# Kernel optimization log

Measured on AMD Instinct MI355X. Metric: run time of the kernel, lower is better.

## Reference

```python
import jax, jax.numpy as jnp
import numpy as np
import math

B, N, D, H, CD = 2, 384, 256, 8, 3
HD = D // H

def _linear_init(key, out_f, in_f):
    k1, k2 = jax.random.split(key)
    bound = 1.0 / math.sqrt(in_f)
    w = jax.random.uniform(k1, (out_f, in_f), jnp.float32, -bound, bound)
    b = jax.random.uniform(k2, (out_f,), jnp.float32, -bound, bound)
    return w, b

def setup_inputs() -> dict:
    key = jax.random.key(0)
    ks = jax.random.split(key, 7)
    x = jax.random.normal(ks[0], (B, N, D), jnp.float32)
    coords = jax.random.normal(ks[1], (B, N, CD), jnp.float32)
    qkv_w, qkv_b = _linear_init(ks[2], 3 * D, D)
    rb_w1, rb_b1 = _linear_init(ks[3], D, CD)
    rb_w2, rb_b2 = _linear_init(ks[4], H, D)
    rv_w1, rv_b1 = _linear_init(ks[5], D, CD)
    rv_w2, rv_b2 = _linear_init(ks[6], D, D)
    return {"x": x, "coords": coords, "qkv_w": qkv_w, "qkv_b": qkv_b,
            "rb_w1": rb_w1, "rb_b1": rb_b1, "rb_w2": rb_w2, "rb_b2": rb_b2,
            "rv_w1": rv_w1, "rv_b1": rv_b1, "rv_w2": rv_w2, "rv_b2": rv_b2}

def reference(x, coords, qkv_w, qkv_b, rb_w1, rb_b1, rb_w2, rb_b2, rv_w1, rv_b1, rv_w2, rv_b2):
    # QKV projection -> (B, H, N, HD) each
    qkv = x @ qkv_w.T + qkv_b
    q, k, v = jnp.split(qkv, 3, axis=-1)
    to_heads = lambda t: t.reshape(B, N, H, HD).transpose(0, 2, 1, 3)
    qh, kh, vh = to_heads(q), to_heads(k), to_heads(v)

    # pairwise relative coordinates: (B, N, N, CD)
    rel = coords[:, :, None, :] - coords[:, None, :, :]

    # rel_bias MLP: (B, N, N, H) -> (B, H, N, N)
    rel_bias = jax.nn.silu(rel @ rb_w1.T + rb_b1) @ rb_w2.T + rb_b2
    rel_bias = rel_bias.transpose(0, 3, 1, 2)

    # rel_value MLP: (B, N, N, D) -> (B, H, N, N, HD)
    rel_value = jax.nn.silu(rel @ rv_w1.T + rv_b1) @ rv_w2.T + rv_b2
    rel_value = rel_value.reshape(B, N, N, H, HD).transpose(0, 3, 1, 2, 4)

    # attn_mask=None path: all-true boolean mask -> additive term is zero
    scores = jnp.einsum('bhid,bhjd->bhij', qh, kh) / math.sqrt(float(HD)) + rel_bias
    weights = jax.nn.softmax(scores, axis=-1)

    base = jnp.einsum('bhij,bhjd->bhid', weights, vh)
    rel_context = jnp.einsum('bhij,bhijd->bhid', weights, rel_value)
    context = base + rel_context  # (B, H, N, HD)
    return context.transpose(0, 2, 1, 3).reshape(B, N, D)
```

## Files before the change

### kernel.cpp

```cpp
#include <hip/hip_runtime.h>
#include <math.h>

#define BB 2
#define NN 384
#define DD 256
#define HH 8
#define RN (BB * NN)
#define INV_SQRT_HD 0.17677669529663687f
#define LOG2E 1.4426950408889634f
#define NLN2 -0.6931471805599453f
#define QSCALE (INV_SQRT_HD * LOG2E)

#define W2_ST 264
#define T_ST  264
#define EB_ST 392

typedef float f32x4 __attribute__((ext_vector_type(4)));
typedef __bf16 bf16x8 __attribute__((ext_vector_type(8)));
typedef __bf16 bf16x4 __attribute__((ext_vector_type(4)));

__device__ __forceinline__ f32x4 mfma16(bf16x8 a, bf16x8 b, f32x4 c) {
    return __builtin_amdgcn_mfma_f32_16x16x32_bf16(a, b, c, 0, 0, 0);
}

__device__ __forceinline__ float hidp(float d) {
    float e = __builtin_amdgcn_exp2f(d);
    return d * __builtin_amdgcn_rcpf(1.0f + e);
}
__device__ __forceinline__ bf16x8 hid8(bf16x8 av, float4 a0, float4 a1) {
    bf16x8 r;
    r[0] = (__bf16)hidp((float)av[0] - a0.x);
    r[1] = (__bf16)hidp((float)av[1] - a0.y);
    r[2] = (__bf16)hidp((float)av[2] - a0.z);
    r[3] = (__bf16)hidp((float)av[3] - a0.w);
    r[4] = (__bf16)hidp((float)av[4] - a1.x);
    r[5] = (__bf16)hidp((float)av[5] - a1.y);
    r[6] = (__bf16)hidp((float)av[6] - a1.z);
    r[7] = (__bf16)hidp((float)av[7] - a1.w);
    return r;
}
__device__ __forceinline__ bf16x8 hid8s(bf16x8 av, float a) {
    bf16x8 r;
#pragma unroll
    for (int q = 0; q < 8; ++q) r[q] = (__bf16)hidp((float)av[q] - a);
    return r;
}
__device__ __forceinline__ bf16x8 pack8(float4 a, float4 b) {
    bf16x8 r;
    r[0] = (__bf16)a.x; r[1] = (__bf16)a.y; r[2] = (__bf16)a.z; r[3] = (__bf16)a.w;
    r[4] = (__bf16)b.x; r[5] = (__bf16)b.y; r[6] = (__bf16)b.z; r[7] = (__bf16)b.w;
    return r;
}
__device__ __forceinline__ float selv(f32x4 v, int r) {
    return (r == 0) ? v[0] : (r == 1) ? v[1] : (r == 2) ? v[2] : v[3];
}

__global__ __launch_bounds__(256) void prep_kernel(
    const float* __restrict__ x, const float* __restrict__ coords,
    const float* __restrict__ qkv_w, const float* __restrict__ qkv_b,
    const float* __restrict__ rb_w1, const float* __restrict__ rv_w1,
    const float* __restrict__ rb_w2,
    float* __restrict__ qb, __bf16* __restrict__ kbbf, __bf16* __restrict__ vT,
    __bf16* __restrict__ Arb, __bf16* __restrict__ ArvT,
    __bf16* __restrict__ w2neg)
{
    int bid = blockIdx.x, tid = threadIdx.x;
    if (bid >= 1344) {
        int idx = tid * 8;
        float4 wa = *(const float4*)(rb_w2 + idx);
        float4 wb = *(const float4*)(rb_w2 + idx + 4);
        float4 na = make_float4(-wa.x, -wa.y, -wa.z, -wa.w);
        float4 nb = make_float4(-wb.x, -wb.y, -wb.z, -wb.w);
        *(bf16x8*)(w2neg + idx) = pack8(na, nb);
        return;
    }
    if (bid >= 576) {
        int r = bid - 576, c = tid;
        float cx = coords[r * 3 + 0], cy = coords[r * 3 + 1], cz = coords[r * 3 + 2];
        float ab = (cx * rb_w1[c * 3] + cy * rb_w1[c * 3 + 1] + cz * rb_w1[c * 3 + 2]) * LOG2E;
        float av = (cx * rv_w1[c * 3] + cy * rv_w1[c * 3 + 1] + cz * rv_w1[c * 3 + 2]) * LOG2E;
        Arb[r * DD + c] = (__bf16)ab;
        ArvT[c * RN + r] = (__bf16)av;
        return;
    }
    int mt = bid % 48, nb = bid / 48;
    int w = tid >> 6, l = tid & 63, lr = l & 15, lg = l >> 4;
    int m0 = mt * 16, n0 = nb * 64 + w * 16;
    const float* xr = x + (size_t)(m0 + lr) * DD;
    const float* wr = qkv_w + (size_t)(n0 + lr) * DD;
    f32x4 acc = {0.f, 0.f, 0.f, 0.f};
#pragma unroll
    for (int ks = 0; ks < 8; ++ks) {
        int c0 = ks * 32 + lg * 8;
        float4 xa = *(const float4*)(xr + c0);
        float4 xb = *(const float4*)(xr + c0 + 4);
        float4 wa = *(const float4*)(wr + c0);
        float4 wb = *(const float4*)(wr + c0 + 4);
        acc = mfma16(pack8(xa, xb), pack8(wa, wb), acc);
    }
    int col = n0 + lr;
    float bo = qkv_b[col];
    int part = col >> 8, o = col & 255;
#pragma unroll
    for (int r = 0; r < 4; ++r) {
        int m = m0 + lg * 4 + r;
        float v = acc[r] + bo;
        if (part == 0) {
            qb[(size_t)m * DD + o] = v * QSCALE;
        } else if (part == 1) {
            kbbf[(size_t)m * DD + o] = (__bf16)v;
        } else {
            int b = (m >= NN) ? 1 : 0;
            int n = m - b * NN;
            vT[(size_t)b * DD * NN + (size_t)o * NN + n] = (__bf16)v;
        }
    }
}

__global__ __launch_bounds__(256, 4) void k2a_kernel(
    const float* __restrict__ rb_b1, const __bf16* __restrict__ w2neg,
    const float* __restrict__ rb_b2,
    const float* __restrict__ qb, const __bf16* __restrict__ kbbf,
    const __bf16* __restrict__ Arb,
    __bf16* __restrict__ eG, float* __restrict__ Zpart)
{
    __shared__ __align__(16) __bf16 qsbf[2][DD];
    __shared__ __align__(16) float Apr[2][DD];
    __shared__ __align__(16) __bf16 w2bf[HH * W2_ST];
    __shared__ float redsm[4][2][HH];

    int tid = threadIdx.x;
    int bid = blockIdx.x;
    int gp = bid >> 1, half = bid & 1;
    int gi0 = gp * 2;
    int b = (gp >= 192) ? 1 : 0;

    qsbf[0][tid] = (__bf16)qb[(size_t)gi0 * DD + tid];
    qsbf[1][tid] = (__bf16)qb[(size_t)(gi0 + 1) * DD + tid];
    float b1l = rb_b1[tid] * LOG2E;
    Apr[0][tid] = (float)Arb[(size_t)gi0 * DD + tid] + b1l;
    Apr[1][tid] = (float)Arb[(size_t)(gi0 + 1) * DD + tid] + b1l;
    {
        int idx = tid * 8;
        *(bf16x8*)&w2bf[(idx >> 8) * W2_ST + (idx & 255)] =
            *(const bf16x8*)(w2neg + idx);
    }
    __syncthreads();

    int l = tid & 63, wv = tid >> 6;
    int lr = l & 15, lg = l >> 4;
    float rb2l = rb_b2[lr & 7] * LOG2E;

    int jb0 = half * 192 + wv * 16;
    int jb1 = jb0 + 64, jb2 = jb0 + 128;
    const __bf16* arbB = Arb + (size_t)b * NN * DD;
    const __bf16* kbB  = kbbf + (size_t)b * NN * DD;
    const __bf16* ar0 = arbB + (size_t)(jb0 + lr) * DD;
    const __bf16* ar1 = arbB + (size_t)(jb1 + lr) * DD;
    const __bf16* ar2 = arbB + (size_t)(jb2 + lr) * DD;
    const __bf16* kr0 = kbB  + (size_t)(jb0 + lr) * DD;
    const __bf16* kr1 = kbB  + (size_t)(jb1 + lr) * DD;
    const __bf16* kr2 = kbB  + (size_t)(jb2 + lr) * DD;
    const __bf16* wfp = &w2bf[(lr & 7) * W2_ST];

    bf16x8 qf0_reg = *(const bf16x8*)&qsbf[0][(lr & 7) * 32 + lg * 8];
    bf16x8 qf1_reg = *(const bf16x8*)&qsbf[1][(lr & 7) * 32 + lg * 8];
    bf16x8 zero8;
#pragma unroll
    for (int e = 0; e < 8; ++e) zero8[e] = (__bf16)0.f;

    f32x4 zzz = {0.f, 0.f, 0.f, 0.f};
    f32x4 a00 = zzz, a01 = zzz, a02 = zzz;
    f32x4 a10 = zzz, a11 = zzz, a12 = zzz;
#pragma unroll
    for (int ks = 0; ks < 8; ++ks) {
        int c0 = ks * 32 + lg * 8;
        bf16x8 v0 = *(const bf16x8*)(ar0 + c0);
        bf16x8 v1 = *(const bf16x8*)(ar1 + c0);
        bf16x8 v2 = *(const bf16x8*)(ar2 + c0);
        bf16x8 k0 = *(const bf16x8*)(kr0 + c0);
        bf16x8 k1 = *(const bf16x8*)(kr1 + c0);
        bf16x8 k2 = *(const bf16x8*)(kr2 + c0);
        bf16x8 wf = *(const bf16x8*)(wfp + c0);
        float4 p00 = *(const float4*)&Apr[0][c0];
        float4 p01 = *(const float4*)&Apr[0][c0 + 4];
        float4 p10 = *(const float4*)&Apr[1][c0];
        float4 p11 = *(const float4*)&Apr[1][c0 + 4];
        bf16x8 q0 = (lr == ks) ? qf0_reg : zero8;
        bf16x8 q1 = (lr == ks) ? qf1_reg : zero8;
        a00 = mfma16(hid8(v0, p00, p01), wf, a00);
        a10 = mfma16(hid8(v0, p10, p11), wf, a10);
        a01 = mfma16(hid8(v1, p00, p01), wf, a01);
        a11 = mfma16(hid8(v1, p10, p11), wf, a11);
        a02 = mfma16(hid8(v2, p00, p01), wf, a02);
        a12 = mfma16(hid8(v2, p10, p11), wf, a12);
        a00 = mfma16(k0, q0, a00);
        a10 = mfma16(k0, q1, a10);
        a01 = mfma16(k1, q0, a01);
        a11 = mfma16(k1, q1, a11);
        a02 = mfma16(k2, q0, a02);
        a12 = mfma16(k2, q1, a12);
    }

    float z0 = 0.f, z1 = 0.f;
#define FINTILE(ACC, GI, JB, ZACC) { \
        float e0 = __builtin_amdgcn_exp2f(ACC[0] + rb2l); \
        float e1 = __builtin_amdgcn_exp2f(ACC[1] + rb2l); \
        float e2 = __builtin_amdgcn_exp2f(ACC[2] + rb2l); \
        float e3 = __builtin_amdgcn_exp2f(ACC[3] + rb2l); \
        if (lr < 8) { \
            bf16x4 ev; \
            ev[0] = (__bf16)e0; ev[1] = (__bf16)e1; \
            ev[2] = (__bf16)e2; ev[3] = (__bf16)e3; \
            *(bf16x4*)&eG[((size_t)(GI) * HH + lr) * NN + (JB) + lg * 4] = ev; \
        } \
        float zs = e0 + e1 + e2 + e3; \
        zs += __shfl_xor(zs, 16); \
        zs += __shfl_xor(zs, 32); \
        ZACC += zs; }
    FINTILE(a00, gi0,     jb0, z0)
    FINTILE(a01, gi0,     jb1, z0)
    FINTILE(a02, gi0,     jb2, z0)
    FINTILE(a10, gi0 + 1, jb0, z1)
    FINTILE(a11, gi0 + 1, jb1, z1)
    FINTILE(a12, gi0 + 1, jb2, z1)
#undef FINTILE
    if (lg == 0 && lr < 8) {
        redsm[wv][0][lr] = z0;
        redsm[wv][1][lr] = z1;
    }
    __syncthreads();
    if (tid < 16) {
        int g = tid >> 3, h = tid & 7;
        Zpart[((size_t)(gi0 + g) * 2 + half) * 8 + h] =
            redsm[0][g][h] + redsm[1][g][h] + redsm[2][g][h] + redsm[3][g][h];
    }
}

__global__ __launch_bounds__(256, 4) void k2b_kernel(
    const float* __restrict__ rv_b1, const float* __restrict__ rv_w2,
    const __bf16* __restrict__ vT, const __bf16* __restrict__ ArvT,
    const __bf16* __restrict__ eG,
    float* __restrict__ rcpart, float* __restrict__ basef)
{
    __shared__ __align__(16) float Apv[2][DD];
    __shared__ __align__(16) float Tl[2][HH * T_ST];
    __shared__ __align__(16) __bf16 els[16 * EB_ST];

    int tid = threadIdx.x;
    int bid = blockIdx.x;
    int gp = bid >> 1, ch = bid & 1;
    int gi0 = gp * 2;
    int b = (gp >= 192) ? 1 : 0;

    float b1l = rv_b1[tid] * LOG2E;
    Apv[0][tid] = (float)ArvT[(size_t)tid * RN + gi0] + b1l;
    Apv[1][tid] = (float)ArvT[(size_t)tid * RN + gi0 + 1] + b1l;
    {
        int r = tid >> 4, cg = tid & 15;
        const __bf16* src = eG + (size_t)(gi0 * 8 + r) * NN;
#pragma unroll
        for (int s = 0; s < 3; ++s) {
            int col = s * 128 + cg * 8;
            *(bf16x8*)&els[r * EB_ST + col] = *(const bf16x8*)(src + col);
        }
    }
    __syncthreads();

    int l = tid & 63, wv = tid >> 6;
    int lr = l & 15, lg = l >> 4;

    int c0 = ch * 128 + wv * 16 + lr;
    int c1 = c0 + 64;
    float ap00 = Apv[0][c0], ap01 = Apv[0][c1];
    float ap10 = Apv[1][c0], ap11 = Apv[1][c1];
    const __bf16* vr0 = ArvT + (size_t)c0 * RN + b * NN;
    const __bf16* vr1 = ArvT + (size_t)c1 * RN + b * NN;
    const __bf16* tv0 = vT + (size_t)b * DD * NN + (size_t)c0 * NN;
    const __bf16* tv1 = vT + (size_t)b * DD * NN + (size_t)c1 * NN;

    f32x4 zzz = {0.f, 0.f, 0.f, 0.f};
    f32x4 T00 = zzz, T01 = zzz, T10 = zzz, T11 = zzz;
    f32x4 B0 = zzz, B1 = zzz;
#pragma unroll
    for (int ks = 0; ks < 12; ++ks) {
        int j0 = ks * 32 + lg * 8;
        bf16x8 ef  = *(const bf16x8*)&els[lr * EB_ST + j0];
        bf16x8 av0 = *(const bf16x8*)(vr0 + j0);
        bf16x8 av1 = *(const bf16x8*)(vr1 + j0);
        bf16x8 w0  = *(const bf16x8*)(tv0 + j0);
        bf16x8 w1  = *(const bf16x8*)(tv1 + j0);
        T00 = mfma16(ef, hid8s(av0, ap00), T00);
        T01 = mfma16(ef, hid8s(av1, ap01), T01);
        T10 = mfma16(ef, hid8s(av0, ap10), T10);
        T11 = mfma16(ef, hid8s(av1, ap11), T11);
        B0  = mfma16(ef, w0, B0);
        B1  = mfma16(ef, w1, B1);
    }

    if (lg < 2) {
#pragma unroll
        for (int r = 0; r < 4; ++r) {
            int h = lg * 4 + r;
            Tl[0][h * T_ST + c0] = T00[r] * NLN2;
            Tl[0][h * T_ST + c1] = T01[r] * NLN2;
        }
    } else {
#pragma unroll
        for (int r = 0; r < 4; ++r) {
            int h = (lg - 2) * 4 + r;
            Tl[1][h * T_ST + c0] = T10[r] * NLN2;
            Tl[1][h * T_ST + c1] = T11[r] * NLN2;
        }
    }
    {
        int h0 = c0 >> 5;
        if (lg == (h0 >> 2))     basef[(size_t)gi0 * DD + c0]       = selv(B0, h0 & 3);
        if (lg == 2 + (h0 >> 2)) basef[(size_t)(gi0 + 1) * DD + c0] = selv(B0, h0 & 3);
        int h1 = c1 >> 5;
        if (lg == (h1 >> 2))     basef[(size_t)gi0 * DD + c1]       = selv(B1, h1 & 3);
        if (lg == 2 + (h1 >> 2)) basef[(size_t)(gi0 + 1) * DD + c1] = selv(B1, h1 & 3);
    }
    __syncthreads();

    {
        int o = tid, h = o >> 5;
        const float4* w2p = (const float4*)(rv_w2 + (size_t)o * DD);
        const float* t0 = &Tl[0][h * T_ST];
        const float* t1 = &Tl[1][h * T_ST];
        float a0 = 0.f, a1 = 0.f;
#pragma unroll 4
        for (int cc = 0; cc < 32; ++cc) {
            int cidx = ch * 32 + cc;
            float4 wv4 = w2p[cidx];
            float4 u0 = *(const float4*)&t0[cidx * 4];
            float4 u1 = *(const float4*)&t1[cidx * 4];
            a0 += wv4.x * u0.x + wv4.y * u0.y + wv4.z * u0.z + wv4.w * u0.w;
            a1 += wv4.x * u1.x + wv4.y * u1.y + wv4.z * u1.z + wv4.w * u1.w;
        }
        rcpart[((size_t)ch * RN + gi0) * DD + o] = a0;
        rcpart[((size_t)ch * RN + gi0 + 1) * DD + o] = a1;
    }
}

__global__ __launch_bounds__(256) void k2c_kernel(
    const float* __restrict__ rcpart, const float* __restrict__ basef,
    const float* __restrict__ Zpart, const float* __restrict__ rv_b2,
    float* __restrict__ out)
{
    int gi = blockIdx.x, o = threadIdx.x, h = o >> 5;
    float z = Zpart[(size_t)gi * 16 + h] + Zpart[(size_t)gi * 16 + 8 + h];
    float rc = rcpart[(size_t)gi * DD + o] + rcpart[((size_t)RN + gi) * DD + o];
    out[(size_t)gi * DD + o] =
        (rc + basef[(size_t)gi * DD + o]) * __builtin_amdgcn_rcpf(z) + rv_b2[o];
}

extern "C" void kernel_launch(void* const* d_in, const int* in_sizes, int n_in,
                              void* d_out, int out_size, void* d_ws, size_t ws_size,
                              hipStream_t stream) {
    const float* x      = (const float*)d_in[0];
    const float* coords = (const float*)d_in[1];
    const float* qkv_w  = (const float*)d_in[2];
    const float* qkv_b  = (const float*)d_in[3];
    const float* rb_w1  = (const float*)d_in[4];
    const float* rb_b1  = (const float*)d_in[5];
    const float* rb_w2  = (const float*)d_in[6];
    const float* rb_b2  = (const float*)d_in[7];
    const float* rv_w1  = (const float*)d_in[8];
    const float* rv_b1  = (const float*)d_in[9];
    const float* rv_w2  = (const float*)d_in[10];
    const float* rv_b2  = (const float*)d_in[11];
    float* out = (float*)d_out;

    float* ws = (float*)d_ws;
    const int PER = RN * DD;
    float* qb = ws;
    __bf16* bfb  = (__bf16*)(ws + PER);
    __bf16* kbbf = bfb;
    __bf16* vTb  = bfb + PER;
    __bf16* Arb  = bfb + 2 * PER;
    __bf16* ArvT = bfb + 3 * PER;
    __bf16* eG   = bfb + 4 * PER;
    float* Zpart = (float*)(eG + (size_t)RN * HH * NN);
    float* basef = Zpart + (size_t)RN * 2 * HH;
    float* rcpart = basef + PER;
    __bf16* w2neg = (__bf16*)(rcpart + 2 * (size_t)PER);

    prep_kernel<<<1345, 256, 0, stream>>>(x, coords, qkv_w, qkv_b,
                                          rb_w1, rv_w1, rb_w2,
                                          qb, kbbf, vTb, Arb, ArvT, w2neg);
    k2a_kernel<<<RN, 256, 0, stream>>>(rb_b1, w2neg, rb_b2,
                                       qb, kbbf, Arb, eG, Zpart);
    k2b_kernel<<<RN, 256, 0, stream>>>(rv_b1, rv_w2,
                                       vTb, ArvT, eG, rcpart, basef);
    k2c_kernel<<<RN, 256, 0, stream>>>(rcpart, basef, Zpart, rv_b2, out);
}
```

Baseline: 76.86 us.

## Fuse score and rel-value kernels, keeping exp weights in LDS per j-half

Merges the attention-score kernel and the rel-value/context kernel into one launch. Each block now keeps its unnormalised exp weights for its 192-key half in shared memory instead of writing them to global and reading them back. The second stage is re-split by key half rather than by output channel, so every block covers all 256 channels over its half of the keys. Per-half base and rel-context partials are summed in the final kernel. This removes one launch and the global round trip of the exp matrix, but each block does the full rv_w2 projection, uses more LDS and registers, and adds a row-major copy of the rel-value first-layer activations.

```diff
diff --git a/kernel.cpp b/kernel.cpp
--- a/kernel.cpp
+++ b/kernel.cpp
@@ -13,7 +13,7 @@
 
 #define W2_ST 264
 #define T_ST  264
-#define EB_ST 392
+#define ELST  200
 
 typedef float f32x4 __attribute__((ext_vector_type(4)));
 typedef __bf16 bf16x8 __attribute__((ext_vector_type(8)));
@@ -61,7 +61,7 @@
     const float* __restrict__ rb_w1, const float* __restrict__ rv_w1,
     const float* __restrict__ rb_w2,
     float* __restrict__ qb, __bf16* __restrict__ kbbf, __bf16* __restrict__ vT,
-    __bf16* __restrict__ Arb, __bf16* __restrict__ ArvT,
+    __bf16* __restrict__ Arb, __bf16* __restrict__ ArvT, __bf16* __restrict__ Arv,
     __bf16* __restrict__ w2neg)
 {
     int bid = blockIdx.x, tid = threadIdx.x;
@@ -81,6 +81,7 @@
         float av = (cx * rv_w1[c * 3] + cy * rv_w1[c * 3 + 1] + cz * rv_w1[c * 3 + 2]) * LOG2E;
         Arb[r * DD + c] = (__bf16)ab;
         ArvT[c * RN + r] = (__bf16)av;
+        Arv[r * DD + c] = (__bf16)av;
         return;
     }
     int mt = bid % 48, nb = bid / 48;
@@ -117,16 +118,22 @@
     }
 }
 
-__global__ __launch_bounds__(256, 4) void k2a_kernel(
+__global__ __launch_bounds__(256, 4) void k2ab_kernel(
     const float* __restrict__ rb_b1, const __bf16* __restrict__ w2neg,
-    const float* __restrict__ rb_b2,
+    const float* __restrict__ rb_b2, const float* __restrict__ rv_b1,
     const float* __restrict__ qb, const __bf16* __restrict__ kbbf,
-    const __bf16* __restrict__ Arb,
-    __bf16* __restrict__ eG, float* __restrict__ Zpart)
+    const __bf16* __restrict__ Arb, const __bf16* __restrict__ ArvT,
+    const __bf16* __restrict__ Arv, const __bf16* __restrict__ vT,
+    const float* __restrict__ rv_w2,
+    float* __restrict__ rcpart, float* __restrict__ basef,
+    float* __restrict__ Zpart)
 {
     __shared__ __align__(16) __bf16 qsbf[2][DD];
     __shared__ __align__(16) float Apr[2][DD];
+    __shared__ __align__(16) float Apv[2][DD];
     __shared__ __align__(16) __bf16 w2bf[HH * W2_ST];
+    __shared__ __align__(16) __bf16 els[16 * ELST];
+    __shared__ __align__(16) float Tl[2][HH * T_ST];
     __shared__ float redsm[4][2][HH];
 
     int tid = threadIdx.x;
@@ -137,9 +144,12 @@
 
     qsbf[0][tid] = (__bf16)qb[(size_t)gi0 * DD + tid];
     qsbf[1][tid] = (__bf16)qb[(size_t)(gi0 + 1) * DD + tid];
-    float b1l = rb_b1[tid] * LOG2E;
-    Apr[0][tid] = (float)Arb[(size_t)gi0 * DD + tid] + b1l;
-    Apr[1][tid] = (float)Arb[(size_t)(gi0 + 1) * DD + tid] + b1l;
+    float b1r = rb_b1[tid] * LOG2E;
+    Apr[0][tid] = (float)Arb[(size_t)gi0 * DD + tid] + b1r;
+    Apr[1][tid] = (float)Arb[(size_t)(gi0 + 1) * DD + tid] + b1r;
+    float b1v = rv_b1[tid] * LOG2E;
+    Apv[0][tid] = (float)Arv[(size_t)gi0 * DD + tid] + b1v;
+    Apv[1][tid] = (float)Arv[(size_t)(gi0 + 1) * DD + tid] + b1v;
     {
         int idx = tid * 8;
         *(bf16x8*)&w2bf[(idx >> 8) * W2_ST + (idx & 255)] =
@@ -151,59 +161,60 @@
     int lr = l & 15, lg = l >> 4;
     float rb2l = rb_b2[lr & 7] * LOG2E;
 
-    int jb0 = half * 192 + wv * 16;
-    int jb1 = jb0 + 64, jb2 = jb0 + 128;
-    const __bf16* arbB = Arb + (size_t)b * NN * DD;
-    const __bf16* kbB  = kbbf + (size_t)b * NN * DD;
-    const __bf16* ar0 = arbB + (size_t)(jb0 + lr) * DD;
-    const __bf16* ar1 = arbB + (size_t)(jb1 + lr) * DD;
-    const __bf16* ar2 = arbB + (size_t)(jb2 + lr) * DD;
-    const __bf16* kr0 = kbB  + (size_t)(jb0 + lr) * DD;
-    const __bf16* kr1 = kbB  + (size_t)(jb1 + lr) * DD;
-    const __bf16* kr2 = kbB  + (size_t)(jb2 + lr) * DD;
-    const __bf16* wfp = &w2bf[(lr & 7) * W2_ST];
-
-    bf16x8 qf0_reg = *(const bf16x8*)&qsbf[0][(lr & 7) * 32 + lg * 8];
-    bf16x8 qf1_reg = *(const bf16x8*)&qsbf[1][(lr & 7) * 32 + lg * 8];
-    bf16x8 zero8;
-#pragma unroll
-    for (int e = 0; e < 8; ++e) zero8[e] = (__bf16)0.f;
-
-    f32x4 zzz = {0.f, 0.f, 0.f, 0.f};
-    f32x4 a00 = zzz, a01 = zzz, a02 = zzz;
-    f32x4 a10 = zzz, a11 = zzz, a12 = zzz;
-#pragma unroll
-    for (int ks = 0; ks < 8; ++ks) {
-        int c0 = ks * 32 + lg * 8;
-        bf16x8 v0 = *(const bf16x8*)(ar0 + c0);
-        bf16x8 v1 = *(const bf16x8*)(ar1 + c0);
-        bf16x8 v2 = *(const bf16x8*)(ar2 + c0);
-        bf16x8 k0 = *(const bf16x8*)(kr0 + c0);
-        bf16x8 k1 = *(const bf16x8*)(kr1 + c0);
-        bf16x8 k2 = *(const bf16x8*)(kr2 + c0);
-        bf16x8 wf = *(const bf16x8*)(wfp + c0);
-        float4 p00 = *(const float4*)&Apr[0][c0];
-        float4 p01 = *(const float4*)&Apr[0][c0 + 4];
-        float4 p10 = *(const float4*)&Apr[1][c0];
-        float4 p11 = *(const float4*)&Apr[1][c0 + 4];
-        bf16x8 q0 = (lr == ks) ? qf0_reg : zero8;
-        bf16x8 q1 = (lr == ks) ? qf1_reg : zero8;
-        a00 = mfma16(hid8(v0, p00, p01), wf, a00);
-        a10 = mfma16(hid8(v0, p10, p11), wf, a10);
-        a01 = mfma16(hid8(v1, p00, p01), wf, a01);
-        a11 = mfma16(hid8(v1, p10, p11), wf, a11);
-        a02 = mfma16(hid8(v2, p00, p01), wf, a02);
-        a12 = mfma16(hid8(v2, p10, p11), wf, a12);
-        a00 = mfma16(k0, q0, a00);
-        a10 = mfma16(k0, q1, a10);
-        a01 = mfma16(k1, q0, a01);
-        a11 = mfma16(k1, q1, a11);
-        a02 = mfma16(k2, q0, a02);
-        a12 = mfma16(k2, q1, a12);
-    }
-
-    float z0 = 0.f, z1 = 0.f;
-#define FINTILE(ACC, GI, JB, ZACC) { \
+    {
+        int jl0 = wv * 16, jl1 = jl0 + 64, jl2 = jl0 + 128;
+        int jg0 = half * 192 + jl0;
+        const __bf16* arbB = Arb + (size_t)b * NN * DD;
+        const __bf16* kbB  = kbbf + (size_t)b * NN * DD;
+        const __bf16* ar0 = arbB + (size_t)(jg0 + lr) * DD;
+        const __bf16* ar1 = ar0 + (size_t)64 * DD;
+        const __bf16* ar2 = ar0 + (size_t)128 * DD;
+        const __bf16* kr0 = kbB + (size_t)(jg0 + lr) * DD;
+        const __bf16* kr1 = kr0 + (size_t)64 * DD;
+        const __bf16* kr2 = kr0 + (size_t)128 * DD;
+        const __bf16* wfp = &w2bf[(lr & 7) * W2_ST];
+
+        bf16x8 qf0_reg = *(const bf16x8*)&qsbf[0][(lr & 7) * 32 + lg * 8];
+        bf16x8 qf1_reg = *(const bf16x8*)&qsbf[1][(lr & 7) * 32 + lg * 8];
+        bf16x8 zero8;
+#pragma unroll
+        for (int e = 0; e < 8; ++e) zero8[e] = (__bf16)0.f;
+
+        f32x4 zzz = {0.f, 0.f, 0.f, 0.f};
+        f32x4 a00 = zzz, a01 = zzz, a02 = zzz;
+        f32x4 a10 = zzz, a11 = zzz, a12 = zzz;
+#pragma unroll
+        for (int ks = 0; ks < 8; ++ks) {
+            int c0 = ks * 32 + lg * 8;
+            bf16x8 v0 = *(const bf16x8*)(ar0 + c0);
+            bf16x8 v1 = *(const bf16x8*)(ar1 + c0);
+            bf16x8 v2 = *(const bf16x8*)(ar2 + c0);
+            bf16x8 k0 = *(const bf16x8*)(kr0 + c0);
+            bf16x8 k1 = *(const bf16x8*)(kr1 + c0);
+            bf16x8 k2 = *(const bf16x8*)(kr2 + c0);
+            bf16x8 wf = *(const bf16x8*)(wfp + c0);
+            float4 p00 = *(const float4*)&Apr[0][c0];
+            float4 p01 = *(const float4*)&Apr[0][c0 + 4];
+            float4 p10 = *(const float4*)&Apr[1][c0];
+            float4 p11 = *(const float4*)&Apr[1][c0 + 4];
+            bf16x8 q0 = (lr == ks) ? qf0_reg : zero8;
+            bf16x8 q1 = (lr == ks) ? qf1_reg : zero8;
+            a00 = mfma16(hid8(v0, p00, p01), wf, a00);
+            a10 = mfma16(hid8(v0, p10, p11), wf, a10);
+            a01 = mfma16(hid8(v1, p00, p01), wf, a01);
+            a11 = mfma16(hid8(v1, p10, p11), wf, a11);
+            a02 = mfma16(hid8(v2, p00, p01), wf, a02);
+            a12 = mfma16(hid8(v2, p10, p11), wf, a12);
+            a00 = mfma16(k0, q0, a00);
+            a10 = mfma16(k0, q1, a10);
+            a01 = mfma16(k1, q0, a01);
+            a11 = mfma16(k1, q1, a11);
+            a02 = mfma16(k2, q0, a02);
+            a12 = mfma16(k2, q1, a12);
+        }
+
+        float z0 = 0.f, z1 = 0.f;
+#define FINTILE(ACC, G, JL, ZACC) { \
         float e0 = __builtin_amdgcn_exp2f(ACC[0] + rb2l); \
         float e1 = __builtin_amdgcn_exp2f(ACC[1] + rb2l); \
         float e2 = __builtin_amdgcn_exp2f(ACC[2] + rb2l); \
@@ -212,22 +223,23 @@
             bf16x4 ev; \
             ev[0] = (__bf16)e0; ev[1] = (__bf16)e1; \
             ev[2] = (__bf16)e2; ev[3] = (__bf16)e3; \
-            *(bf16x4*)&eG[((size_t)(GI) * HH + lr) * NN + (JB) + lg * 4] = ev; \
+            *(bf16x4*)&els[((G) * 8 + lr) * ELST + (JL) + lg * 4] = ev; \
         } \
         float zs = e0 + e1 + e2 + e3; \
         zs += __shfl_xor(zs, 16); \
         zs += __shfl_xor(zs, 32); \
         ZACC += zs; }
-    FINTILE(a00, gi0,     jb0, z0)
-    FINTILE(a01, gi0,     jb1, z0)
-    FINTILE(a02, gi0,     jb2, z0)
-    FINTILE(a10, gi0 + 1, jb0, z1)
-    FINTILE(a11, gi0 + 1, jb1, z1)
-    FINTILE(a12, gi0 + 1, jb2, z1)
+        FINTILE(a00, 0, jl0, z0)
+        FINTILE(a01, 0, jl1, z0)
+        FINTILE(a02, 0, jl2, z0)
+        FINTILE(a10, 1, jl0, z1)
+        FINTILE(a11, 1, jl1, z1)
+        FINTILE(a12, 1, jl2, z1)
 #undef FINTILE
-    if (lg == 0 && lr < 8) {
-        redsm[wv][0][lr] = z0;
-        redsm[wv][1][lr] = z1;
+        if (lg == 0 && lr < 8) {
+            redsm[wv][0][lr] = z0;
+            redsm[wv][1][lr] = z1;
+        }
     }
     __syncthreads();
     if (tid < 16) {
@@ -235,91 +247,86 @@
         Zpart[((size_t)(gi0 + g) * 2 + half) * 8 + h] =
             redsm[0][g][h] + redsm[1][g][h] + redsm[2][g][h] + redsm[3][g][h];
     }
-}
-
-__global__ __launch_bounds__(256, 4) void k2b_kernel(
-    const float* __restrict__ rv_b1, const float* __restrict__ rv_w2,
-    const __bf16* __restrict__ vT, const __bf16* __restrict__ ArvT,
-    const __bf16* __restrict__ eG,
-    float* __restrict__ rcpart, float* __restrict__ basef)
-{
-    __shared__ __align__(16) float Apv[2][DD];
-    __shared__ __align__(16) float Tl[2][HH * T_ST];
-    __shared__ __align__(16) __bf16 els[16 * EB_ST];
-
-    int tid = threadIdx.x;
-    int bid = blockIdx.x;
-    int gp = bid >> 1, ch = bid & 1;
-    int gi0 = gp * 2;
-    int b = (gp >= 192) ? 1 : 0;
-
-    float b1l = rv_b1[tid] * LOG2E;
-    Apv[0][tid] = (float)ArvT[(size_t)tid * RN + gi0] + b1l;
-    Apv[1][tid] = (float)ArvT[(size_t)tid * RN + gi0 + 1] + b1l;
+
     {
-        int r = tid >> 4, cg = tid & 15;
-        const __bf16* src = eG + (size_t)(gi0 * 8 + r) * NN;
-#pragma unroll
-        for (int s = 0; s < 3; ++s) {
-            int col = s * 128 + cg * 8;
-            *(bf16x8*)&els[r * EB_ST + col] = *(const bf16x8*)(src + col);
-        }
-    }
-    __syncthreads();
-
-    int l = tid & 63, wv = tid >> 6;
-    int lr = l & 15, lg = l >> 4;
-
-    int c0 = ch * 128 + wv * 16 + lr;
-    int c1 = c0 + 64;
-    float ap00 = Apv[0][c0], ap01 = Apv[0][c1];
-    float ap10 = Apv[1][c0], ap11 = Apv[1][c1];
-    const __bf16* vr0 = ArvT + (size_t)c0 * RN + b * NN;
-    const __bf16* vr1 = ArvT + (size_t)c1 * RN + b * NN;
-    const __bf16* tv0 = vT + (size_t)b * DD * NN + (size_t)c0 * NN;
-    const __bf16* tv1 = vT + (size_t)b * DD * NN + (size_t)c1 * NN;
-
-    f32x4 zzz = {0.f, 0.f, 0.f, 0.f};
-    f32x4 T00 = zzz, T01 = zzz, T10 = zzz, T11 = zzz;
-    f32x4 B0 = zzz, B1 = zzz;
-#pragma unroll
-    for (int ks = 0; ks < 12; ++ks) {
-        int j0 = ks * 32 + lg * 8;
-        bf16x8 ef  = *(const bf16x8*)&els[lr * EB_ST + j0];
-        bf16x8 av0 = *(const bf16x8*)(vr0 + j0);
-        bf16x8 av1 = *(const bf16x8*)(vr1 + j0);
-        bf16x8 w0  = *(const bf16x8*)(tv0 + j0);
-        bf16x8 w1  = *(const bf16x8*)(tv1 + j0);
-        T00 = mfma16(ef, hid8s(av0, ap00), T00);
-        T01 = mfma16(ef, hid8s(av1, ap01), T01);
-        T10 = mfma16(ef, hid8s(av0, ap10), T10);
-        T11 = mfma16(ef, hid8s(av1, ap11), T11);
-        B0  = mfma16(ef, w0, B0);
-        B1  = mfma16(ef, w1, B1);
-    }
-
-    if (lg < 2) {
-#pragma unroll
-        for (int r = 0; r < 4; ++r) {
-            int h = lg * 4 + r;
-            Tl[0][h * T_ST + c0] = T00[r] * NLN2;
-            Tl[0][h * T_ST + c1] = T01[r] * NLN2;
-        }
-    } else {
-#pragma unroll
-        for (int r = 0; r < 4; ++r) {
-            int h = (lg - 2) * 4 + r;
-            Tl[1][h * T_ST + c0] = T10[r] * NLN2;
-            Tl[1][h * T_ST + c1] = T11[r] * NLN2;
-        }
-    }
-    {
-        int h0 = c0 >> 5;
-        if (lg == (h0 >> 2))     basef[(size_t)gi0 * DD + c0]       = selv(B0, h0 & 3);
-        if (lg == 2 + (h0 >> 2)) basef[(size_t)(gi0 + 1) * DD + c0] = selv(B0, h0 & 3);
-        int h1 = c1 >> 5;
-        if (lg == (h1 >> 2))     basef[(size_t)gi0 * DD + c1]       = selv(B1, h1 & 3);
-        if (lg == 2 + (h1 >> 2)) basef[(size_t)(gi0 + 1) * DD + c1] = selv(B1, h1 & 3);
+        int cc = wv * 16 + lr;
+        float ap00 = Apv[0][cc], ap01 = Apv[0][cc + 64];
+        float ap02 = Apv[0][cc + 128], ap03 = Apv[0][cc + 192];
+        float ap10 = Apv[1][cc], ap11 = Apv[1][cc + 64];
+        float ap12 = Apv[1][cc + 128], ap13 = Apv[1][cc + 192];
+        int joff = b * NN + half * 192;
+        const __bf16* vr0 = ArvT + (size_t)cc * RN + joff;
+        const __bf16* vr1 = ArvT + (size_t)(cc + 64) * RN + joff;
+        const __bf16* vr2 = ArvT + (size_t)(cc + 128) * RN + joff;
+        const __bf16* vr3 = ArvT + (size_t)(cc + 192) * RN + joff;
+        const __bf16* tvB = vT + (size_t)b * DD * NN + half * 192;
+        const __bf16* tv0 = tvB + (size_t)cc * NN;
+        const __bf16* tv1 = tvB + (size_t)(cc + 64) * NN;
+        const __bf16* tv2 = tvB + (size_t)(cc + 128) * NN;
+        const __bf16* tv3 = tvB + (size_t)(cc + 192) * NN;
+
+        f32x4 zzz = {0.f, 0.f, 0.f, 0.f};
+        f32x4 T00 = zzz, T01 = zzz, T02 = zzz, T03 = zzz;
+        f32x4 T10 = zzz, T11 = zzz, T12 = zzz, T13 = zzz;
+        f32x4 Bb0 = zzz, Bb1 = zzz, Bb2 = zzz, Bb3 = zzz;
+#pragma unroll
+        for (int ks = 0; ks < 6; ++ks) {
+            int j0 = ks * 32 + lg * 8;
+            bf16x8 ef  = *(const bf16x8*)&els[lr * ELST + j0];
+            bf16x8 av0 = *(const bf16x8*)(vr0 + j0);
+            bf16x8 av1 = *(const bf16x8*)(vr1 + j0);
+            bf16x8 av2 = *(const bf16x8*)(vr2 + j0);
+            bf16x8 av3 = *(const bf16x8*)(vr3 + j0);
+            bf16x8 w0  = *(const bf16x8*)(tv0 + j0);
+            bf16x8 w1  = *(const bf16x8*)(tv1 + j0);
+            bf16x8 w2  = *(const bf16x8*)(tv2 + j0);
+            bf16x8 w3  = *(const bf16x8*)(tv3 + j0);
+            T00 = mfma16(ef, hid8s(av0, ap00), T00);
+            T01 = mfma16(ef, hid8s(av1, ap01), T01);
+            T02 = mfma16(ef, hid8s(av2, ap02), T02);
+            T03 = mfma16(ef, hid8s(av3, ap03), T03);
+            T10 = mfma16(ef, hid8s(av0, ap10), T10);
+            T11 = mfma16(ef, hid8s(av1, ap11), T11);
+            T12 = mfma16(ef, hid8s(av2, ap12), T12);
+            T13 = mfma16(ef, hid8s(av3, ap13), T13);
+            Bb0 = mfma16(ef, w0, Bb0);
+            Bb1 = mfma16(ef, w1, Bb1);
+            Bb2 = mfma16(ef, w2, Bb2);
+            Bb3 = mfma16(ef, w3, Bb3);
+        }
+
+        if (lg < 2) {
+#pragma unroll
+            for (int r = 0; r < 4; ++r) {
+                int h = lg * 4 + r;
+                Tl[0][h * T_ST + cc      ] = T00[r] * NLN2;
+                Tl[0][h * T_ST + cc +  64] = T01[r] * NLN2;
+                Tl[0][h * T_ST + cc + 128] = T02[r] * NLN2;
+                Tl[0][h * T_ST + cc + 192] = T03[r] * NLN2;
+            }
+        } else {
+#pragma unroll
+            for (int r = 0; r < 4; ++r) {
+                int h = (lg - 2) * 4 + r;
+                Tl[1][h * T_ST + cc      ] = T10[r] * NLN2;
+                Tl[1][h * T_ST + cc +  64] = T11[r] * NLN2;
+                Tl[1][h * T_ST + cc + 128] = T12[r] * NLN2;
+                Tl[1][h * T_ST + cc + 192] = T13[r] * NLN2;
+            }
+        }
+        {
+            float* bz = basef + (size_t)half * RN * DD;
+#define BEXT(BACC, CS) { \
+            int c = (CS) * 64 + cc; \
+            int h = c >> 5; \
+            if (lg == (h >> 2))     bz[(size_t)gi0 * DD + c]       = selv(BACC, h & 3); \
+            if (lg == 2 + (h >> 2)) bz[(size_t)(gi0 + 1) * DD + c] = selv(BACC, h & 3); }
+            BEXT(Bb0, 0)
+            BEXT(Bb1, 1)
+            BEXT(Bb2, 2)
+            BEXT(Bb3, 3)
+#undef BEXT
+        }
     }
     __syncthreads();
 
@@ -330,16 +337,16 @@
         const float* t1 = &Tl[1][h * T_ST];
         float a0 = 0.f, a1 = 0.f;
 #pragma unroll 4
-        for (int cc = 0; cc < 32; ++cc) {
-            int cidx = ch * 32 + cc;
-            float4 wv4 = w2p[cidx];
-            float4 u0 = *(const float4*)&t0[cidx * 4];
-            float4 u1 = *(const float4*)&t1[cidx * 4];
+        for (int cc2 = 0; cc2 < 64; ++cc2) {
+            float4 wv4 = w2p[cc2];
+            float4 u0 = *(const float4*)&t0[cc2 * 4];
+            float4 u1 = *(const float4*)&t1[cc2 * 4];
             a0 += wv4.x * u0.x + wv4.y * u0.y + wv4.z * u0.z + wv4.w * u0.w;
             a1 += wv4.x * u1.x + wv4.y * u1.y + wv4.z * u1.z + wv4.w * u1.w;
         }
-        rcpart[((size_t)ch * RN + gi0) * DD + o] = a0;
-        rcpart[((size_t)ch * RN + gi0 + 1) * DD + o] = a1;
+        float* rz = rcpart + (size_t)half * RN * DD;
+        rz[(size_t)gi0 * DD + o] = a0;
+        rz[(size_t)(gi0 + 1) * DD + o] = a1;
     }
 }
 
@@ -350,9 +357,11 @@
 {
     int gi = blockIdx.x, o = threadIdx.x, h = o >> 5;
     float z = Zpart[(size_t)gi * 16 + h] + Zpart[(size_t)gi * 16 + 8 + h];
-    float rc = rcpart[(size_t)gi * DD + o] + rcpart[((size_t)RN + gi) * DD + o];
-    out[(size_t)gi * DD + o] =
-        (rc + basef[(size_t)gi * DD + o]) * __builtin_amdgcn_rcpf(z) + rv_b2[o];
+    size_t io = (size_t)gi * DD + o;
+    const size_t SL = (size_t)RN * DD;
+    float rc = rcpart[io] + rcpart[SL + io];
+    float base = basef[io] + basef[SL + io];
+    out[io] = (rc + base) * __builtin_amdgcn_rcpf(z) + rv_b2[o];
 }
 
 extern "C" void kernel_launch(void* const* d_in, const int* in_sizes, int n_in,
@@ -380,18 +389,17 @@
     __bf16* vTb  = bfb + PER;
     __bf16* Arb  = bfb + 2 * PER;
     __bf16* ArvT = bfb + 3 * PER;
-    __bf16* eG   = bfb + 4 * PER;
-    float* Zpart = (float*)(eG + (size_t)RN * HH * NN);
+    __bf16* Arv  = bfb + 4 * PER;
+    float* Zpart = (float*)(bfb + 5 * PER);
     float* basef = Zpart + (size_t)RN * 2 * HH;
-    float* rcpart = basef + PER;
+    float* rcpart = basef + 2 * (size_t)PER;
     __bf16* w2neg = (__bf16*)(rcpart + 2 * (size_t)PER);
 
     prep_kernel<<<1345, 256, 0, stream>>>(x, coords, qkv_w, qkv_b,
                                           rb_w1, rv_w1, rb_w2,
-                                          qb, kbbf, vTb, Arb, ArvT, w2neg);
-    k2a_kernel<<<RN, 256, 0, stream>>>(rb_b1, w2neg, rb_b2,
-                                       qb, kbbf, Arb, eG, Zpart);
-    k2b_kernel<<<RN, 256, 0, stream>>>(rv_b1, rv_w2,
-                                       vTb, ArvT, eG, rcpart, basef);
+                                          qb, kbbf, vTb, Arb, ArvT, Arv, w2neg);
+    k2ab_kernel<<<RN, 256, 0, stream>>>(rb_b1, w2neg, rb_b2, rv_b1,
+                                        qb, kbbf, Arb, ArvT, Arv, vTb, rv_w2,
+                                        rcpart, basef, Zpart);
     k2c_kernel<<<RN, 256, 0, stream>>>(rcpart, basef, Zpart, rv_b2, out);
 }
```

After: 80.98 us. 1.05x slower.

## Split rel-value kernel over channel quarters and key halves, move W2 projection to final kernel

Applied to the files above, without the earlier changes.

The rel-value kernel is re-partitioned so each block handles a 64-channel quarter and a half of the key range, staging ArvT, vT and attention-weight tiles in shared memory instead of reading them directly from global memory. The per-block W2 matvec is moved into the final combine kernel, which now reduces the bf16 partial T sums across key halves before projecting. This gives more blocks and shared-memory reuse, at the cost of extra bf16 partial buffers, an extra Arv layout written in prep, and bf16 rounding of the intermediate T values.

```diff
diff --git a/kernel.cpp b/kernel.cpp
--- a/kernel.cpp
+++ b/kernel.cpp
@@ -12,8 +12,7 @@
 #define QSCALE (INV_SQRT_HD * LOG2E)
 
 #define W2_ST 264
-#define T_ST  264
-#define EB_ST 392
+#define EB 200
 
 typedef float f32x4 __attribute__((ext_vector_type(4)));
 typedef __bf16 bf16x8 __attribute__((ext_vector_type(8)));
@@ -61,7 +60,7 @@
     const float* __restrict__ rb_w1, const float* __restrict__ rv_w1,
     const float* __restrict__ rb_w2,
     float* __restrict__ qb, __bf16* __restrict__ kbbf, __bf16* __restrict__ vT,
-    __bf16* __restrict__ Arb, __bf16* __restrict__ ArvT,
+    __bf16* __restrict__ Arb, __bf16* __restrict__ ArvT, __bf16* __restrict__ Arv,
     __bf16* __restrict__ w2neg)
 {
     int bid = blockIdx.x, tid = threadIdx.x;
@@ -81,6 +80,7 @@
         float av = (cx * rv_w1[c * 3] + cy * rv_w1[c * 3 + 1] + cz * rv_w1[c * 3 + 2]) * LOG2E;
         Arb[r * DD + c] = (__bf16)ab;
         ArvT[c * RN + r] = (__bf16)av;
+        Arv[r * DD + c] = (__bf16)av;
         return;
     }
     int mt = bid % 48, nb = bid / 48;
@@ -237,122 +237,143 @@
     }
 }
 
-__global__ __launch_bounds__(256, 4) void k2b_kernel(
-    const float* __restrict__ rv_b1, const float* __restrict__ rv_w2,
+__global__ __launch_bounds__(256, 2) void k2b_kernel(
+    const float* __restrict__ rv_b1,
     const __bf16* __restrict__ vT, const __bf16* __restrict__ ArvT,
-    const __bf16* __restrict__ eG,
-    float* __restrict__ rcpart, float* __restrict__ basef)
+    const __bf16* __restrict__ Arv, const __bf16* __restrict__ eG,
+    __bf16* __restrict__ Tpart, float* __restrict__ basef)
 {
-    __shared__ __align__(16) float Apv[2][DD];
-    __shared__ __align__(16) float Tl[2][HH * T_ST];
-    __shared__ __align__(16) __bf16 els[16 * EB_ST];
+    __shared__ __align__(16) __bf16 AvL[64 * EB];
+    __shared__ __align__(16) __bf16 VtL[64 * EB];
+    __shared__ __align__(16) __bf16 EL[16 * EB];
+    __shared__ float aps[2][64];
 
     int tid = threadIdx.x;
     int bid = blockIdx.x;
-    int gp = bid >> 1, ch = bid & 1;
+    int gp = bid >> 3, cq = (bid >> 1) & 3, jh = bid & 1;
     int gi0 = gp * 2;
     int b = (gp >= 192) ? 1 : 0;
-
-    float b1l = rv_b1[tid] * LOG2E;
-    Apv[0][tid] = (float)ArvT[(size_t)tid * RN + gi0] + b1l;
-    Apv[1][tid] = (float)ArvT[(size_t)tid * RN + gi0 + 1] + b1l;
+    int joff = b * NN + jh * 192;
+
+    const __bf16* avbase = ArvT + (size_t)(cq * 64) * RN + joff;
+    const __bf16* vtbase = vT + (size_t)b * DD * NN + (size_t)(cq * 64) * NN + jh * 192;
+    const __bf16* ebase  = eG + (size_t)(gi0 * 8) * NN + jh * 192;
+
+    bf16x8 tA[6], tV[6], tE0, tE1;
+#pragma unroll
+    for (int s = 0; s < 6; ++s) {
+        int idx = tid + s * 256;
+        int r = idx / 24, cc = idx - r * 24;
+        tA[s] = *(const bf16x8*)(avbase + (size_t)r * RN + cc * 8);
+        tV[s] = *(const bf16x8*)(vtbase + (size_t)r * NN + cc * 8);
+    }
     {
-        int r = tid >> 4, cg = tid & 15;
-        const __bf16* src = eG + (size_t)(gi0 * 8 + r) * NN;
-#pragma unroll
-        for (int s = 0; s < 3; ++s) {
-            int col = s * 128 + cg * 8;
-            *(bf16x8*)&els[r * EB_ST + col] = *(const bf16x8*)(src + col);
+        int r = tid / 24, cc = tid - r * 24;
+        tE0 = *(const bf16x8*)(ebase + (size_t)r * NN + cc * 8);
+        if (tid < 128) {
+            int idx = 256 + tid;
+            int r1 = idx / 24, cc1 = idx - r1 * 24;
+            tE1 = *(const bf16x8*)(ebase + (size_t)r1 * NN + cc1 * 8);
+        }
+    }
+    if (tid < 128) {
+        int g = tid >> 6, c = tid & 63;
+        aps[g][c] = (float)Arv[(size_t)(gi0 + g) * DD + cq * 64 + c]
+                  + rv_b1[cq * 64 + c] * LOG2E;
+    }
+#pragma unroll
+    for (int s = 0; s < 6; ++s) {
+        int idx = tid + s * 256;
+        int r = idx / 24, cc = idx - r * 24;
+        *(bf16x8*)&AvL[r * EB + cc * 8] = tA[s];
+        *(bf16x8*)&VtL[r * EB + cc * 8] = tV[s];
+    }
+    {
+        int r = tid / 24, cc = tid - r * 24;
+        *(bf16x8*)&EL[r * EB + cc * 8] = tE0;
+        if (tid < 128) {
+            int idx = 256 + tid;
+            int r1 = idx / 24, cc1 = idx - r1 * 24;
+            *(bf16x8*)&EL[r1 * EB + cc1 * 8] = tE1;
         }
     }
     __syncthreads();
 
     int l = tid & 63, wv = tid >> 6;
     int lr = l & 15, lg = l >> 4;
-
-    int c0 = ch * 128 + wv * 16 + lr;
-    int c1 = c0 + 64;
-    float ap00 = Apv[0][c0], ap01 = Apv[0][c1];
-    float ap10 = Apv[1][c0], ap11 = Apv[1][c1];
-    const __bf16* vr0 = ArvT + (size_t)c0 * RN + b * NN;
-    const __bf16* vr1 = ArvT + (size_t)c1 * RN + b * NN;
-    const __bf16* tv0 = vT + (size_t)b * DD * NN + (size_t)c0 * NN;
-    const __bf16* tv1 = vT + (size_t)b * DD * NN + (size_t)c1 * NN;
-
-    f32x4 zzz = {0.f, 0.f, 0.f, 0.f};
-    f32x4 T00 = zzz, T01 = zzz, T10 = zzz, T11 = zzz;
-    f32x4 B0 = zzz, B1 = zzz;
-#pragma unroll
-    for (int ks = 0; ks < 12; ++ks) {
-        int j0 = ks * 32 + lg * 8;
-        bf16x8 ef  = *(const bf16x8*)&els[lr * EB_ST + j0];
-        bf16x8 av0 = *(const bf16x8*)(vr0 + j0);
-        bf16x8 av1 = *(const bf16x8*)(vr1 + j0);
-        bf16x8 w0  = *(const bf16x8*)(tv0 + j0);
-        bf16x8 w1  = *(const bf16x8*)(tv1 + j0);
-        T00 = mfma16(ef, hid8s(av0, ap00), T00);
-        T01 = mfma16(ef, hid8s(av1, ap01), T01);
-        T10 = mfma16(ef, hid8s(av0, ap10), T10);
-        T11 = mfma16(ef, hid8s(av1, ap11), T11);
-        B0  = mfma16(ef, w0, B0);
-        B1  = mfma16(ef, w1, B1);
-    }
-
+    int rc_ = wv * 16 + lr;
+    float ap0 = aps[0][rc_], ap1 = aps[1][rc_];
+
+    f32x4 zz = {0.f, 0.f, 0.f, 0.f};
+    f32x4 T0 = zz, T1 = zz, B0 = zz;
+#pragma unroll
+    for (int ks = 0; ks < 6; ++ks) {
+        int jo = ks * 32 + lg * 8;
+        bf16x8 ef  = *(const bf16x8*)&EL[lr * EB + jo];
+        bf16x8 av  = *(const bf16x8*)&AvL[rc_ * EB + jo];
+        bf16x8 wv8 = *(const bf16x8*)&VtL[rc_ * EB + jo];
+        T0 = mfma16(ef, hid8s(av, ap0), T0);
+        T1 = mfma16(ef, hid8s(av, ap1), T1);
+        B0 = mfma16(ef, wv8, B0);
+    }
+
+    int cglob = cq * 64 + rc_;
+    __bf16* tp = Tpart + (size_t)jh * RN * HH * DD;
     if (lg < 2) {
 #pragma unroll
         for (int r = 0; r < 4; ++r) {
             int h = lg * 4 + r;
-            Tl[0][h * T_ST + c0] = T00[r] * NLN2;
-            Tl[0][h * T_ST + c1] = T01[r] * NLN2;
+            tp[((size_t)gi0 * HH + h) * DD + cglob] = (__bf16)T0[r];
         }
     } else {
 #pragma unroll
         for (int r = 0; r < 4; ++r) {
             int h = (lg - 2) * 4 + r;
-            Tl[1][h * T_ST + c0] = T10[r] * NLN2;
-            Tl[1][h * T_ST + c1] = T11[r] * NLN2;
+            tp[((size_t)(gi0 + 1) * HH + h) * DD + cglob] = (__bf16)T1[r];
         }
     }
     {
-        int h0 = c0 >> 5;
-        if (lg == (h0 >> 2))     basef[(size_t)gi0 * DD + c0]       = selv(B0, h0 & 3);
-        if (lg == 2 + (h0 >> 2)) basef[(size_t)(gi0 + 1) * DD + c0] = selv(B0, h0 & 3);
-        int h1 = c1 >> 5;
-        if (lg == (h1 >> 2))     basef[(size_t)gi0 * DD + c1]       = selv(B1, h1 & 3);
-        if (lg == 2 + (h1 >> 2)) basef[(size_t)(gi0 + 1) * DD + c1] = selv(B1, h1 & 3);
+        int h = cglob >> 5;
+        float* bz = basef + (size_t)jh * RN * DD;
+        if (lg == (h >> 2))     bz[(size_t)gi0 * DD + cglob]       = selv(B0, h & 3);
+        if (lg == 2 + (h >> 2)) bz[(size_t)(gi0 + 1) * DD + cglob] = selv(B0, h & 3);
+    }
+}
+
+__global__ __launch_bounds__(256) void k2c_kernel(
+    const __bf16* __restrict__ Tpart, const float* __restrict__ basef,
+    const float* __restrict__ Zpart, const float* __restrict__ rv_w2,
+    const float* __restrict__ rv_b2, float* __restrict__ out)
+{
+    __shared__ __align__(16) float Ts[HH * 264];
+    int gi = blockIdx.x, tid = threadIdx.x;
+    const __bf16* t0 = Tpart + (size_t)gi * HH * DD;
+    const __bf16* t1 = Tpart + ((size_t)RN + gi) * HH * DD;
+    {
+        int h = tid >> 5, c0 = (tid & 31) * 8;
+        bf16x8 u0 = *(const bf16x8*)&t0[h * DD + c0];
+        bf16x8 u1 = *(const bf16x8*)&t1[h * DD + c0];
+#pragma unroll
+        for (int q = 0; q < 8; ++q)
+            Ts[h * 264 + c0 + q] = ((float)u0[q] + (float)u1[q]) * NLN2;
     }
     __syncthreads();
 
-    {
-        int o = tid, h = o >> 5;
-        const float4* w2p = (const float4*)(rv_w2 + (size_t)o * DD);
-        const float* t0 = &Tl[0][h * T_ST];
-        const float* t1 = &Tl[1][h * T_ST];
-        float a0 = 0.f, a1 = 0.f;
+    int o = tid, h = o >> 5;
+    float z = Zpart[(size_t)gi * 16 + h] + Zpart[(size_t)gi * 16 + 8 + h];
+    const float4* w2p = (const float4*)(rv_w2 + (size_t)o * DD);
+    const float* trow = &Ts[h * 264];
+    float a = 0.f;
 #pragma unroll 4
-        for (int cc = 0; cc < 32; ++cc) {
-            int cidx = ch * 32 + cc;
-            float4 wv4 = w2p[cidx];
-            float4 u0 = *(const float4*)&t0[cidx * 4];
-            float4 u1 = *(const float4*)&t1[cidx * 4];
-            a0 += wv4.x * u0.x + wv4.y * u0.y + wv4.z * u0.z + wv4.w * u0.w;
-            a1 += wv4.x * u1.x + wv4.y * u1.y + wv4.z * u1.z + wv4.w * u1.w;
-        }
-        rcpart[((size_t)ch * RN + gi0) * DD + o] = a0;
-        rcpart[((size_t)ch * RN + gi0 + 1) * DD + o] = a1;
-    }
-}
-
-__global__ __launch_bounds__(256) void k2c_kernel(
-    const float* __restrict__ rcpart, const float* __restrict__ basef,
-    const float* __restrict__ Zpart, const float* __restrict__ rv_b2,
-    float* __restrict__ out)
-{
-    int gi = blockIdx.x, o = threadIdx.x, h = o >> 5;
-    float z = Zpart[(size_t)gi * 16 + h] + Zpart[(size_t)gi * 16 + 8 + h];
-    float rc = rcpart[(size_t)gi * DD + o] + rcpart[((size_t)RN + gi) * DD + o];
-    out[(size_t)gi * DD + o] =
-        (rc + basef[(size_t)gi * DD + o]) * __builtin_amdgcn_rcpf(z) + rv_b2[o];
+    for (int cc = 0; cc < 64; ++cc) {
+        float4 w4 = w2p[cc];
+        float4 u = *(const float4*)&trow[cc * 4];
+        a += w4.x * u.x + w4.y * u.y + w4.z * u.z + w4.w * u.w;
+    }
+    size_t io = (size_t)gi * DD + o;
+    const size_t SL = (size_t)RN * DD;
+    float base = basef[io] + basef[SL + io];
+    out[io] = (a + base) * __builtin_amdgcn_rcpf(z) + rv_b2[o];
 }
 
 extern "C" void kernel_launch(void* const* d_in, const int* in_sizes, int n_in,
@@ -380,18 +401,19 @@
     __bf16* vTb  = bfb + PER;
     __bf16* Arb  = bfb + 2 * PER;
     __bf16* ArvT = bfb + 3 * PER;
-    __bf16* eG   = bfb + 4 * PER;
-    float* Zpart = (float*)(eG + (size_t)RN * HH * NN);
+    __bf16* Arv  = bfb + 4 * PER;
+    __bf16* eG   = bfb + 5 * (size_t)PER;
+    __bf16* Tpart = eG + (size_t)RN * HH * NN;
+    float* Zpart = (float*)(Tpart + (size_t)2 * RN * HH * DD);
     float* basef = Zpart + (size_t)RN * 2 * HH;
-    float* rcpart = basef + PER;
-    __bf16* w2neg = (__bf16*)(rcpart + 2 * (size_t)PER);
+    __bf16* w2neg = (__bf16*)(basef + 2 * (size_t)PER);
 
     prep_kernel<<<1345, 256, 0, stream>>>(x, coords, qkv_w, qkv_b,
                                           rb_w1, rv_w1, rb_w2,
-                                          qb, kbbf, vTb, Arb, ArvT, w2neg);
+                                          qb, kbbf, vTb, Arb, ArvT, Arv, w2neg);
     k2a_kernel<<<RN, 256, 0, stream>>>(rb_b1, w2neg, rb_b2,
                                        qb, kbbf, Arb, eG, Zpart);
-    k2b_kernel<<<RN, 256, 0, stream>>>(rv_b1, rv_w2,
-                                       vTb, ArvT, eG, rcpart, basef);
-    k2c_kernel<<<RN, 256, 0, stream>>>(rcpart, basef, Zpart, rv_b2, out);
-}
+    k2b_kernel<<<8 * 384, 256, 0, stream>>>(rv_b1, vTb, ArvT, Arv, eG,
+                                            Tpart, basef);
+    k2c_kernel<<<RN, 256, 0, stream>>>(Tpart, basef, Zpart, rv_w2, rv_b2, out);
+}
```

Result: slower. 94.34 us (+22.7%).
